# Optimization experiments

Measured on AMD Instinct MI355X. Metric: run time of the kernel, lower is better.

Reference implementation:

```python
import jax, jax.numpy as jnp
import numpy as np

SOS = 0
EOS = 1
NEG = -10000.0
B, S, T = 128, 1024, 128


def setup_inputs() -> dict:
    key = jax.random.key(0)
    k1, k2, k3 = jax.random.split(key, 3)
    emissions = jax.random.normal(k1, (B, S, T), dtype=jnp.float32)
    tags = jax.random.randint(k2, (B, S), 0, T)
    mask = jnp.ones((B, S), dtype=jnp.float32)
    transition = jax.random.uniform(k3, (T, T), minval=-0.1, maxval=0.1, dtype=jnp.float32)
    transition = transition.at[:, SOS].set(NEG).at[EOS, :].set(NEG)
    return {"emissions": emissions, "transition": transition, "mask": mask, "tags": tags}


def _crf_nll(emissions, transition, mask, tags):
    b, s, t = emissions.shape
    barange = jnp.arange(b)

    # ---- gold-path score (vectorized over time) ----
    first_tags = tags[:, 0]
    last_valid_idx = mask.astype(jnp.int32).sum(1) - 1
    last_tags = jnp.take_along_axis(tags, last_valid_idx[:, None], axis=1)[:, 0]

    score = transition[SOS, first_tags] + emissions[:, 0][barange, first_tags]
    e_scores = jnp.take_along_axis(emissions, tags[:, :, None], axis=2)[:, :, 0]  # (B,S)
    t_scores = transition[tags[:, :-1], tags[:, 1:]]                              # (B,S-1)
    score = score + ((e_scores[:, 1:] + t_scores) * mask[:, 1:]).sum(axis=1)
    score = score + transition[last_tags, EOS]

    # ---- log partition via forward algorithm (lax.scan over time) ----
    alphas0 = transition[SOS][None, :] + emissions[:, 0]  # (B,T)

    def step(alphas, inp):
        e_i, m_i = inp  # (B,T), (B,)
        # scores[b, prev, cur] = alphas[b, prev] + transition[prev, cur] + e_i[b, cur]
        scores = alphas[:, :, None] + transition[None, :, :] + e_i[:, None, :]
        new_alphas = jax.scipy.special.logsumexp(scores, axis=1)  # (B,T)
        m = m_i[:, None]
        return m * new_alphas + (1.0 - m) * alphas, None

    em_t = jnp.swapaxes(emissions, 0, 1)[1:]  # (S-1, B, T)
    mk_t = mask.T[1:]                         # (S-1, B)
    alphas, _ = jax.lax.scan(step, alphas0, (em_t, mk_t))

    partition = jax.scipy.special.logsumexp(alphas + transition[:, EOS][None, :], axis=1)  # (B,)
    return -jnp.sum(score - partition)


def reference(emissions, transition, mask, tags):
    return _crf_nll(emissions, transition, mask, tags)
```

## Files before the change

### kernel.cpp

```cpp
#include <hip/hip_runtime.h>
#include <cmath>

#define SOS 0
#define EOS 1
#define Bb 128
#define Ss 1024
#define Tt 128
#define LOG2E 1.4426950408889634f
#define LN2f  0.6931471805599453f

__global__ __launch_bounds__(256) void crf_forward(
    const float* __restrict__ em, const float* __restrict__ trans,
    const float* __restrict__ mask, float* __restrict__ part_out)
{
  __shared__ __align__(16) float s_trans[Tt * Tt];
  __shared__ __align__(16) float s_f[2][Tt];
  __shared__ __align__(16) float s_red[4];
  __shared__ __align__(16) float s_mask[Ss];

  const int tid = threadIdx.x;
  const int w   = tid >> 6;
  const int l   = tid & 63;
  const int jl  = l & 31;
  const int j   = w * 32 + jl;
  const int kh  = l >> 5;
  const int kbase = kh * 64;
  const int b   = blockIdx.x;
  const size_t base = (size_t)b * Ss * Tt;

  for (int i = tid; i < Ss; i += 256) s_mask[i] = mask[b * Ss + i];
  #pragma unroll
  for (int it = 0; it < 16; ++it) {
    int idx = (it * 256 + tid) * 4;
    *(float4*)&s_trans[idx] = *(const float4*)&trans[idx];
  }
  if (tid < 4) s_red[tid] = 0.5f;
  __syncthreads();

  float Mreg[64];
  #pragma unroll
  for (int kk = 0; kk < 64; ++kk)
    Mreg[kk] = exp2f(s_trans[(kbase + kk) * Tt + j] * LOG2E);
  const float tSOS  = s_trans[SOS * Tt + j];
  const float tEOS2 = s_trans[j * Tt + EOS] * LOG2E;

  float fn = exp2f((tSOS + em[base + j]) * LOG2E);
  if (l < 32) s_f[0][j] = fn;
  float c_scale = 0.f;
  float em0 = em[base + (size_t)1 * Tt + j];
  float em1 = em[base + (size_t)2 * Tt + j];
  __syncthreads();

  for (int i = 1; i < Ss; ++i) {
    const int p = i & 1;
    int ip = (i + 2 < Ss) ? (i + 2) : (Ss - 1);
    float em2 = em[base + (size_t)ip * Tt + j];
    float mi = s_mask[i];
    float fold = s_f[p ^ 1][j];

    float scl = 1.0f;
    if ((i & 3) == 1) {
      float4 r4 = *(float4*)&s_red[0];
      float M = fmaxf(fmaxf(r4.x, r4.y), fmaxf(r4.z, r4.w));
      int e; (void)frexpf(M, &e);
      scl = __int_as_float((127 - e) << 23);
      c_scale += (float)e;
    }
    float w_ = exp2f(em0 * LOG2E) * scl;

    float acc0 = 0.f, acc1 = 0.f, acc2 = 0.f, acc3 = 0.f;
    const float4* fsrc = (const float4*)&s_f[p ^ 1][kbase];
    #pragma unroll
    for (int q = 0; q < 16; ++q) {
      float4 fv = fsrc[q];
      acc0 = fmaf(fv.x, Mreg[4 * q + 0], acc0);
      acc1 = fmaf(fv.y, Mreg[4 * q + 1], acc1);
      acc2 = fmaf(fv.z, Mreg[4 * q + 2], acc2);
      acc3 = fmaf(fv.w, Mreg[4 * q + 3], acc3);
    }
    float g = (acc0 + acc1) + (acc2 + acc3);
    g += __shfl_xor(g, 32);

    float fnew = g * w_;
    fold *= scl;
    fn = (mi == 0.f) ? fold : fnew;
    if (l < 32) s_f[p][j] = fn;

    if ((i & 3) == 0) {
      float v = fn;
      #pragma unroll
      for (int o = 16; o > 0; o >>= 1) v = fmaxf(v, __shfl_xor(v, o));
      if (l == 0) s_red[w] = v;
    }
    em0 = em1; em1 = em2;
    __syncthreads();
  }

  float v = (l < 32) ? fn * exp2f(tEOS2) : 0.f;
  #pragma unroll
  for (int o = 32; o > 0; o >>= 1) v += __shfl_xor(v, o);
  if (l == 0) s_red[w] = v;
  __syncthreads();
  if (tid == 0) {
    float s = (s_red[0] + s_red[1]) + (s_red[2] + s_red[3]);
    part_out[b] = (log2f(s) + c_scale) * LN2f;
  }
}

__global__ __launch_bounds__(256) void crf_score(
    const float* __restrict__ em, const float* __restrict__ trans,
    const float* __restrict__ mask, const int* __restrict__ tags,
    float* __restrict__ sc)
{
  __shared__ float s_red[4];
  __shared__ float s_red2[4];
  const int tid = threadIdx.x;
  const int b = blockIdx.x;
  const size_t em_base = (size_t)b * Ss * Tt;
  const int* tg = tags + b * Ss;
  const float* mk = mask + b * Ss;

  float part = 0.f, msum = 0.f;
  for (int i = tid; i < Ss; i += 256) {
    float m = mk[i];
    msum += m;
    if (i >= 1) {
      int tc = tg[i], tp = tg[i - 1];
      part += m * (em[em_base + (size_t)i * Tt + tc] + trans[tp * Tt + tc]);
    }
  }
  #pragma unroll
  for (int o = 32; o > 0; o >>= 1) {
    part += __shfl_xor(part, o);
    msum += __shfl_xor(msum, o);
  }
  if ((tid & 63) == 0) { s_red[tid >> 6] = part; s_red2[tid >> 6] = msum; }
  __syncthreads();
  if (tid == 0) {
    float p  = s_red[0] + s_red[1] + s_red[2] + s_red[3];
    float ms = s_red2[0] + s_red2[1] + s_red2[2] + s_red2[3];
    int last = (int)(ms + 0.5f) - 1;
    int t0 = tg[0];
    float s = trans[SOS * Tt + t0] + em[em_base + t0] + p
            + trans[tg[last] * Tt + EOS];
    sc[b] = s;
  }
}

__global__ __launch_bounds__(128) void crf_combine(
    const float* __restrict__ part, const float* __restrict__ sc,
    float* __restrict__ out)
{
  __shared__ float s_red[2];
  const int tid = threadIdx.x;
  float v = part[tid] - sc[tid];
  #pragma unroll
  for (int o = 32; o > 0; o >>= 1) v += __shfl_xor(v, o);
  if ((tid & 63) == 0) s_red[tid >> 6] = v;
  __syncthreads();
  if (tid == 0) out[0] = s_red[0] + s_red[1];
}

extern "C" void kernel_launch(void* const* d_in, const int* in_sizes, int n_in,
                              void* d_out, int out_size, void* d_ws, size_t ws_size,
                              hipStream_t stream)
{
  const float* em    = (const float*)d_in[0];
  const float* trans = (const float*)d_in[1];
  const float* mask  = (const float*)d_in[2];
  const int*   tags  = (const int*)d_in[3];
  float* out = (float*)d_out;
  float* wsf = (float*)d_ws;
  float* part = wsf;
  float* sc   = wsf + 128;

  hipLaunchKernelGGL(crf_score, dim3(Bb), dim3(256), 0, stream,
                     em, trans, mask, tags, sc);
  hipLaunchKernelGGL(crf_forward, dim3(Bb), dim3(256), 0, stream,
                     em, trans, mask, part);
  hipLaunchKernelGGL(crf_combine, dim3(1), dim3(128), 0, stream,
                     part, sc, out);
}
```

Baseline: 543.3 us.

## Run CRF forward recurrence on a single wavefront with packed FMAs

Shrinks the forward kernel from four wavefronts to one 64-lane wavefront per sequence. Each lane keeps two output columns of the exponentiated transition matrix in registers and computes them with v_pk_fma_f32. This removes the per-step __syncthreads, the cross-half shuffle and the shared-memory max reduction, and the rescale max now uses only intra-wave shuffles. In exchange each lane does four times the multiply-adds per step, holds about 256 VGPRs of matrix data, and relies on LDS ordering within one wave for correctness.

```diff
diff --git a/kernel.cpp b/kernel.cpp
--- a/kernel.cpp
+++ b/kernel.cpp
@@ -9,102 +9,116 @@
 #define LOG2E 1.4426950408889634f
 #define LN2f  0.6931471805599453f
 
-__global__ __launch_bounds__(256) void crf_forward(
+typedef float f32x2 __attribute__((ext_vector_type(2)));
+typedef float f32x4 __attribute__((ext_vector_type(4)));
+
+__device__ __forceinline__ void pkfma(f32x2& acc, f32x2 a, f32x2 b) {
+  asm("v_pk_fma_f32 %0, %1, %2, %0" : "+v"(acc) : "v"(a), "v"(b));
+}
+
+template<int PH>
+__device__ __forceinline__ void crf_step(
+    int i, const float* __restrict__ em, size_t base, int j0,
+    float* s_f, const float* s_mask,
+    const f32x2 (&MA)[64], const f32x2 (&MB)[64],
+    f32x2& fprev, f32x2& pf, float& c_scale, float& nxt_scl, float& nxt_e)
+{
+  *(f32x2*)&s_f[j0] = fprev;
+  float mi = s_mask[i];
+  f32x2 emv = pf;
+  int r = (i + 4 < Ss) ? (i + 4) : (Ss - 1);
+  pf = *(const f32x2*)&em[base + (size_t)r * Tt + j0];
+
+  float sclv = 1.0f;
+  if constexpr (PH == 0) { sclv = nxt_scl; c_scale += nxt_e; }
+
+  f32x2 aA0 = {0.f, 0.f}, aA1 = {0.f, 0.f};
+  f32x2 aB0 = {0.f, 0.f}, aB1 = {0.f, 0.f};
+  const f32x4* fq = (const f32x4*)s_f;
+  #pragma unroll
+  for (int q = 0; q < 32; ++q) {
+    f32x4 v = fq[q];
+    f32x2 lo = __builtin_shufflevector(v, v, 0, 1);
+    f32x2 hi = __builtin_shufflevector(v, v, 2, 3);
+    pkfma(aA0, lo, MA[2 * q]);
+    pkfma(aA1, hi, MA[2 * q + 1]);
+    pkfma(aB0, lo, MB[2 * q]);
+    pkfma(aB1, hi, MB[2 * q + 1]);
+  }
+  f32x2 g;
+  g.x = (aA0.x + aA0.y) + (aA1.x + aA1.y);
+  g.y = (aB0.x + aB0.y) + (aB1.x + aB1.y);
+
+  f32x2 fn;
+  fn.x = g.x * (exp2f(emv.x * LOG2E) * sclv);
+  fn.y = g.y * (exp2f(emv.y * LOG2E) * sclv);
+  if (mi == 0.f) { fn.x = fprev.x * sclv; fn.y = fprev.y * sclv; }
+  fprev = fn;
+
+  if constexpr (PH == 3) {
+    float v = fmaxf(fn.x, fn.y);
+    #pragma unroll
+    for (int o = 32; o > 0; o >>= 1) v = fmaxf(v, __shfl_xor(v, o));
+    int e2; (void)frexpf(v, &e2);
+    nxt_scl = __int_as_float((127 - e2) << 23);
+    nxt_e = (float)e2;
+  }
+}
+
+__global__ __launch_bounds__(64, 1) void crf_forward(
     const float* __restrict__ em, const float* __restrict__ trans,
     const float* __restrict__ mask, float* __restrict__ part_out)
 {
-  __shared__ __align__(16) float s_trans[Tt * Tt];
-  __shared__ __align__(16) float s_f[2][Tt];
-  __shared__ __align__(16) float s_red[4];
+  __shared__ __align__(16) float s_f[Tt];
   __shared__ __align__(16) float s_mask[Ss];
 
-  const int tid = threadIdx.x;
-  const int w   = tid >> 6;
-  const int l   = tid & 63;
-  const int jl  = l & 31;
-  const int j   = w * 32 + jl;
-  const int kh  = l >> 5;
-  const int kbase = kh * 64;
-  const int b   = blockIdx.x;
+  const int l = threadIdx.x;
+  const int j0 = 2 * l;
+  const int b = blockIdx.x;
   const size_t base = (size_t)b * Ss * Tt;
 
-  for (int i = tid; i < Ss; i += 256) s_mask[i] = mask[b * Ss + i];
+  for (int i = l; i < Ss; i += 64) s_mask[i] = mask[b * Ss + i];
+
+  f32x2 MA[64], MB[64];
   #pragma unroll
-  for (int it = 0; it < 16; ++it) {
-    int idx = (it * 256 + tid) * 4;
-    *(float4*)&s_trans[idx] = *(const float4*)&trans[idx];
+  for (int k2 = 0; k2 < 64; ++k2) {
+    f32x2 r0 = *(const f32x2*)&trans[(2 * k2 + 0) * Tt + j0];
+    f32x2 r1 = *(const f32x2*)&trans[(2 * k2 + 1) * Tt + j0];
+    MA[k2] = f32x2{ exp2f(r0.x * LOG2E), exp2f(r1.x * LOG2E) };
+    MB[k2] = f32x2{ exp2f(r0.y * LOG2E), exp2f(r1.y * LOG2E) };
   }
-  if (tid < 4) s_red[tid] = 0.5f;
+  const f32x2 tS = *(const f32x2*)&trans[SOS * Tt + j0];
+  const float eA = exp2f(trans[(j0 + 0) * Tt + EOS] * LOG2E);
+  const float eB = exp2f(trans[(j0 + 1) * Tt + EOS] * LOG2E);
+
+  f32x2 e0 = *(const f32x2*)&em[base + j0];
+  f32x2 fprev;
+  fprev.x = exp2f((tS.x + e0.x) * LOG2E);
+  fprev.y = exp2f((tS.y + e0.y) * LOG2E);
+
+  f32x2 pf1 = *(const f32x2*)&em[base + (size_t)1 * Tt + j0];
+  f32x2 pf2 = *(const f32x2*)&em[base + (size_t)2 * Tt + j0];
+  f32x2 pf3 = *(const f32x2*)&em[base + (size_t)3 * Tt + j0];
+  f32x2 pf0 = *(const f32x2*)&em[base + (size_t)4 * Tt + j0];
+
+  float c_scale = 0.f, nxt_scl = 1.f, nxt_e = 0.f;
   __syncthreads();
 
-  float Mreg[64];
-  #pragma unroll
-  for (int kk = 0; kk < 64; ++kk)
-    Mreg[kk] = exp2f(s_trans[(kbase + kk) * Tt + j] * LOG2E);
-  const float tSOS  = s_trans[SOS * Tt + j];
-  const float tEOS2 = s_trans[j * Tt + EOS] * LOG2E;
+  int i = 1;
+  for (; i + 3 < Ss; i += 4) {
+    crf_step<1>(i + 0, em, base, j0, s_f, s_mask, MA, MB, fprev, pf1, c_scale, nxt_scl, nxt_e);
+    crf_step<2>(i + 1, em, base, j0, s_f, s_mask, MA, MB, fprev, pf2, c_scale, nxt_scl, nxt_e);
+    crf_step<3>(i + 2, em, base, j0, s_f, s_mask, MA, MB, fprev, pf3, c_scale, nxt_scl, nxt_e);
+    crf_step<0>(i + 3, em, base, j0, s_f, s_mask, MA, MB, fprev, pf0, c_scale, nxt_scl, nxt_e);
+  }
+  crf_step<1>(i + 0, em, base, j0, s_f, s_mask, MA, MB, fprev, pf1, c_scale, nxt_scl, nxt_e);
+  crf_step<2>(i + 1, em, base, j0, s_f, s_mask, MA, MB, fprev, pf2, c_scale, nxt_scl, nxt_e);
+  crf_step<3>(i + 2, em, base, j0, s_f, s_mask, MA, MB, fprev, pf3, c_scale, nxt_scl, nxt_e);
 
-  float fn = exp2f((tSOS + em[base + j]) * LOG2E);
-  if (l < 32) s_f[0][j] = fn;
-  float c_scale = 0.f;
-  float em0 = em[base + (size_t)1 * Tt + j];
-  float em1 = em[base + (size_t)2 * Tt + j];
-  __syncthreads();
-
-  for (int i = 1; i < Ss; ++i) {
-    const int p = i & 1;
-    int ip = (i + 2 < Ss) ? (i + 2) : (Ss - 1);
-    float em2 = em[base + (size_t)ip * Tt + j];
-    float mi = s_mask[i];
-    float fold = s_f[p ^ 1][j];
-
-    float scl = 1.0f;
-    if ((i & 3) == 1) {
-      float4 r4 = *(float4*)&s_red[0];
-      float M = fmaxf(fmaxf(r4.x, r4.y), fmaxf(r4.z, r4.w));
-      int e; (void)frexpf(M, &e);
-      scl = __int_as_float((127 - e) << 23);
-      c_scale += (float)e;
-    }
-    float w_ = exp2f(em0 * LOG2E) * scl;
-
-    float acc0 = 0.f, acc1 = 0.f, acc2 = 0.f, acc3 = 0.f;
-    const float4* fsrc = (const float4*)&s_f[p ^ 1][kbase];
-    #pragma unroll
-    for (int q = 0; q < 16; ++q) {
-      float4 fv = fsrc[q];
-      acc0 = fmaf(fv.x, Mreg[4 * q + 0], acc0);
-      acc1 = fmaf(fv.y, Mreg[4 * q + 1], acc1);
-      acc2 = fmaf(fv.z, Mreg[4 * q + 2], acc2);
-      acc3 = fmaf(fv.w, Mreg[4 * q + 3], acc3);
-    }
-    float g = (acc0 + acc1) + (acc2 + acc3);
-    g += __shfl_xor(g, 32);
-
-    float fnew = g * w_;
-    fold *= scl;
-    fn = (mi == 0.f) ? fold : fnew;
-    if (l < 32) s_f[p][j] = fn;
-
-    if ((i & 3) == 0) {
-      float v = fn;
-      #pragma unroll
-      for (int o = 16; o > 0; o >>= 1) v = fmaxf(v, __shfl_xor(v, o));
-      if (l == 0) s_red[w] = v;
-    }
-    em0 = em1; em1 = em2;
-    __syncthreads();
-  }
-
-  float v = (l < 32) ? fn * exp2f(tEOS2) : 0.f;
+  float v = fprev.x * eA + fprev.y * eB;
   #pragma unroll
   for (int o = 32; o > 0; o >>= 1) v += __shfl_xor(v, o);
-  if (l == 0) s_red[w] = v;
-  __syncthreads();
-  if (tid == 0) {
-    float s = (s_red[0] + s_red[1]) + (s_red[2] + s_red[3]);
-    part_out[b] = (log2f(s) + c_scale) * LN2f;
-  }
+  if (l == 0) part_out[b] = (log2f(v) + c_scale) * LN2f;
 }
 
 __global__ __launch_bounds__(256) void crf_score(
@@ -176,7 +190,7 @@
 
   hipLaunchKernelGGL(crf_score, dim3(Bb), dim3(256), 0, stream,
                      em, trans, mask, tags, sc);
-  hipLaunchKernelGGL(crf_forward, dim3(Bb), dim3(256), 0, stream,
+  hipLaunchKernelGGL(crf_forward, dim3(Bb), dim3(64), 0, stream,
                      em, trans, mask, part);
   hipLaunchKernelGGL(crf_combine, dim3(1), dim3(128), 0, stream,
                      part, sc, out);
```

Result: slower. 1.622 ms (+198.6%).

## Split CRF recursion into forward/backward halves using bf16 MFMA batched over sequences

Applied to the files above, without the earlier changes.

Replaces the per-sequence 256-thread FMA forward recursion with a forward-backward split: 32 blocks run the forward recursion over the first half of the sequence and 32 blocks run the backward recursion over the second half. Each block handles 4 sequences at once with the exp-transition matrix held in registers as bf16 MFMA fragments. A new combine kernel dots the alpha and beta vectors. This halves the serial chain length and turns the matvec into matrix-matrix MFMA work. In exchange it uses bf16 precision for the state and transition, runs only 64 single-wave blocks (low occupancy), and adds a kernel launch.

```diff
diff --git a/kernel.cpp b/kernel.cpp
--- a/kernel.cpp
+++ b/kernel.cpp
@@ -1,5 +1,6 @@
 #include <hip/hip_runtime.h>
 #include <cmath>
+#include <stdint.h>
 
 #define SOS 0
 #define EOS 1
@@ -9,102 +10,317 @@
 #define LOG2E 1.4426950408889634f
 #define LN2f  0.6931471805599453f
 
-__global__ __launch_bounds__(256) void crf_forward(
+typedef float  f32x2  __attribute__((ext_vector_type(2)));
+typedef float  f32x4  __attribute__((ext_vector_type(4)));
+typedef short  short4v __attribute__((ext_vector_type(4)));
+typedef short  short8v __attribute__((ext_vector_type(8)));
+
+#define WS_F    0
+#define WS_U    16384
+#define WS_CF   32768
+#define WS_CB   32896
+#define WS_PART 33024
+#define WS_SC   33152
+
+__device__ __forceinline__ unsigned short f2bf(float f) {
+  unsigned u = __float_as_uint(f);
+  return (unsigned short)((u + 0x7FFFu + ((u >> 16) & 1u)) >> 16);
+}
+__device__ __forceinline__ float bf2f(unsigned short h) {
+  return __uint_as_float(((unsigned)h) << 16);
+}
+__device__ __forceinline__ int sigma(int p) {
+  int t = p >> 4, cc = p & 15;
+  return 32 * (t & 3) + 2 * cc + (t >> 2);
+}
+
+template<int PH>
+__device__ __forceinline__ void crf_iter(
+    int it, bool fwd, int b0, int c, int g, bool allones,
+    const float* __restrict__ em, const float* __restrict__ mask,
+    unsigned short* y_s, float (&w_lds)[4][4][136],
+    const short8v (&Bf)[32],
+    f32x4& emE0, f32x4& emE1, f32x4& emO0, f32x4& emO1,
+    float& e_pend, f32x4& c4)
+{
+  constexpr int slot  = PH;
+  constexpr int slot2 = (PH + 2) & 3;
+  const unsigned ybase = (unsigned)(uintptr_t)y_s;
+
+  f32x2 wr[4][4];
+#pragma unroll
+  for (int m = 0; m < 4; ++m)
+#pragma unroll
+    for (int T = 0; T < 4; ++T)
+      wr[m][T] = *(const f32x2*)&w_lds[slot][m][32 * T + 2 * c];
+
+  asm volatile("s_waitcnt lgkmcnt(0)" ::: "memory");
+  short4v t0[4], t1[4];
+#pragma unroll
+  for (int kt = 0; kt < 4; ++kt) {
+    unsigned a1 = ybase + (unsigned)((32 * kt + 4 * g) * 32 + 2 * c);
+    asm volatile("ds_read_b64_tr_b16 %0, %1" : "=v"(t0[kt]) : "v"(a1));
+    asm volatile("ds_read_b64_tr_b16 %0, %1 offset:512" : "=v"(t1[kt]) : "v"(a1));
+  }
+  asm volatile("s_waitcnt lgkmcnt(0)" ::: "memory");
+  __builtin_amdgcn_sched_barrier(0);
+
+  short8v a8[4];
+#pragma unroll
+  for (int kt = 0; kt < 4; ++kt) {
+    short8v v;
+    v[0] = t0[kt][0]; v[1] = t0[kt][1]; v[2] = t0[kt][2]; v[3] = t0[kt][3];
+    v[4] = t1[kt][0]; v[5] = t1[kt][1]; v[6] = t1[kt][2]; v[7] = t1[kt][3];
+    a8[kt] = v;
+  }
+
+  f32x4 acc[8];
+#pragma unroll
+  for (int jt = 0; jt < 8; ++jt) acc[jt] = (f32x4){0.f, 0.f, 0.f, 0.f};
+#pragma unroll
+  for (int kt = 0; kt < 4; ++kt)
+#pragma unroll
+    for (int jt = 0; jt < 8; ++jt)
+      acc[jt] = __builtin_amdgcn_mfma_f32_16x16x32_bf16(a8[kt], Bf[kt * 8 + jt], acc[jt], 0, 0, 0);
+
+  {
+    f32x4 ea, eb2;
+    if constexpr (PH & 1) { ea = emO0; eb2 = emO1; } else { ea = emE0; eb2 = emE1; }
+    const float fold = (PH == 1) ? e_pend : 0.0f;
+    f32x4 wa, wb;
+#pragma unroll
+    for (int q = 0; q < 4; ++q) {
+      wa[q] = __builtin_amdgcn_exp2f(fmaf(ea[q],  LOG2E, -fold));
+      wb[q] = __builtin_amdgcn_exp2f(fmaf(eb2[q], LOG2E, -fold));
+    }
+    float* wp = &w_lds[slot2][g][8 * c];
+    *(f32x4*)wp = wa;
+    *(f32x4*)(wp + 4) = wb;
+    const int lr = fwd ? it + 4 : 1023 - it - 4;
+    const float* p = em + ((size_t)(b0 + g) * Ss + lr) * Tt + 8 * c;
+    f32x4 n0 = *(const f32x4*)p;
+    f32x4 n1 = *(const f32x4*)(p + 4);
+    if constexpr (PH & 1) { emO0 = n0; emO1 = n1; } else { emE0 = n0; emE1 = n1; }
+  }
+
+  float mloc = 0.0f;
+  f32x4 m4 = (f32x4){1.f, 1.f, 1.f, 1.f};
+  if (!allones) {
+    const int wrow = fwd ? it : 1023 - it;
+    m4[0] = mask[(size_t)(b0 + 0) * Ss + wrow];
+    m4[1] = mask[(size_t)(b0 + 1) * Ss + wrow];
+    m4[2] = mask[(size_t)(b0 + 2) * Ss + wrow];
+    m4[3] = mask[(size_t)(b0 + 3) * Ss + wrow];
+  }
+#pragma unroll
+  for (int jt = 0; jt < 8; ++jt) {
+    const int T = jt & 3, hi = jt >> 2;
+    float y0 = acc[jt][0] * wr[0][T][hi];
+    float y1 = acc[jt][1] * wr[1][T][hi];
+    float y2 = acc[jt][2] * wr[2][T][hi];
+    float y3 = acc[jt][3] * wr[3][T][hi];
+    if (!allones) {
+      short4v ov = *(short4v*)&y_s[(16 * jt + c) * 16];
+      if (m4[0] == 0.f) y0 = bf2f((unsigned short)ov[0]);
+      if (m4[1] == 0.f) y1 = bf2f((unsigned short)ov[1]);
+      if (m4[2] == 0.f) y2 = bf2f((unsigned short)ov[2]);
+      if (m4[3] == 0.f) y3 = bf2f((unsigned short)ov[3]);
+    }
+    if constexpr (PH == 0)
+      mloc = fmaxf(fmaxf(fmaxf(mloc, y0), fmaxf(y1, y2)), y3);
+    if (g == 0) {
+      short4v pk;
+      pk[0] = (short)f2bf(y0); pk[1] = (short)f2bf(y1);
+      pk[2] = (short)f2bf(y2); pk[3] = (short)f2bf(y3);
+      *(short4v*)&y_s[(16 * jt + c) * 16] = pk;
+    }
+  }
+  if constexpr (PH == 0) {
+#pragma unroll
+    for (int o = 1; o < 16; o <<= 1) mloc = fmaxf(mloc, __shfl_xor(mloc, o));
+    float g0 = __shfl(mloc, c);
+    int ei = (int)((__float_as_uint(g0) >> 23) & 255u) - 127;
+    e_pend = (float)ei;
+  }
+  if constexpr (PH == 3) {
+    if (allones) {
+      c4[0] += e_pend; c4[1] += e_pend; c4[2] += e_pend; c4[3] += e_pend;
+    } else {
+      c4[0] += (m4[0] != 0.f) ? e_pend : 0.f;
+      c4[1] += (m4[1] != 0.f) ? e_pend : 0.f;
+      c4[2] += (m4[2] != 0.f) ? e_pend : 0.f;
+      c4[3] += (m4[3] != 0.f) ? e_pend : 0.f;
+    }
+  }
+}
+
+__global__ __launch_bounds__(64) void crf_fb(
     const float* __restrict__ em, const float* __restrict__ trans,
-    const float* __restrict__ mask, float* __restrict__ part_out)
+    const float* __restrict__ mask, float* __restrict__ wsf)
 {
   __shared__ __align__(16) float s_trans[Tt * Tt];
-  __shared__ __align__(16) float s_f[2][Tt];
-  __shared__ __align__(16) float s_red[4];
-  __shared__ __align__(16) float s_mask[Ss];
-
-  const int tid = threadIdx.x;
-  const int w   = tid >> 6;
-  const int l   = tid & 63;
-  const int jl  = l & 31;
-  const int j   = w * 32 + jl;
-  const int kh  = l >> 5;
-  const int kbase = kh * 64;
-  const int b   = blockIdx.x;
-  const size_t base = (size_t)b * Ss * Tt;
-
-  for (int i = tid; i < Ss; i += 256) s_mask[i] = mask[b * Ss + i];
-  #pragma unroll
-  for (int it = 0; it < 16; ++it) {
-    int idx = (it * 256 + tid) * 4;
-    *(float4*)&s_trans[idx] = *(const float4*)&trans[idx];
-  }
-  if (tid < 4) s_red[tid] = 0.5f;
-  __syncthreads();
-
-  float Mreg[64];
-  #pragma unroll
-  for (int kk = 0; kk < 64; ++kk)
-    Mreg[kk] = exp2f(s_trans[(kbase + kk) * Tt + j] * LOG2E);
-  const float tSOS  = s_trans[SOS * Tt + j];
-  const float tEOS2 = s_trans[j * Tt + EOS] * LOG2E;
-
-  float fn = exp2f((tSOS + em[base + j]) * LOG2E);
-  if (l < 32) s_f[0][j] = fn;
-  float c_scale = 0.f;
-  float em0 = em[base + (size_t)1 * Tt + j];
-  float em1 = em[base + (size_t)2 * Tt + j];
-  __syncthreads();
-
-  for (int i = 1; i < Ss; ++i) {
-    const int p = i & 1;
-    int ip = (i + 2 < Ss) ? (i + 2) : (Ss - 1);
-    float em2 = em[base + (size_t)ip * Tt + j];
-    float mi = s_mask[i];
-    float fold = s_f[p ^ 1][j];
-
-    float scl = 1.0f;
-    if ((i & 3) == 1) {
-      float4 r4 = *(float4*)&s_red[0];
-      float M = fmaxf(fmaxf(r4.x, r4.y), fmaxf(r4.z, r4.w));
-      int e; (void)frexpf(M, &e);
-      scl = __int_as_float((127 - e) << 23);
-      c_scale += (float)e;
-    }
-    float w_ = exp2f(em0 * LOG2E) * scl;
-
-    float acc0 = 0.f, acc1 = 0.f, acc2 = 0.f, acc3 = 0.f;
-    const float4* fsrc = (const float4*)&s_f[p ^ 1][kbase];
-    #pragma unroll
-    for (int q = 0; q < 16; ++q) {
-      float4 fv = fsrc[q];
-      acc0 = fmaf(fv.x, Mreg[4 * q + 0], acc0);
-      acc1 = fmaf(fv.y, Mreg[4 * q + 1], acc1);
-      acc2 = fmaf(fv.z, Mreg[4 * q + 2], acc2);
-      acc3 = fmaf(fv.w, Mreg[4 * q + 3], acc3);
-    }
-    float g = (acc0 + acc1) + (acc2 + acc3);
-    g += __shfl_xor(g, 32);
-
-    float fnew = g * w_;
-    fold *= scl;
-    fn = (mi == 0.f) ? fold : fnew;
-    if (l < 32) s_f[p][j] = fn;
-
-    if ((i & 3) == 0) {
-      float v = fn;
-      #pragma unroll
-      for (int o = 16; o > 0; o >>= 1) v = fmaxf(v, __shfl_xor(v, o));
-      if (l == 0) s_red[w] = v;
-    }
-    em0 = em1; em1 = em2;
-    __syncthreads();
-  }
-
-  float v = (l < 32) ? fn * exp2f(tEOS2) : 0.f;
-  #pragma unroll
-  for (int o = 32; o > 0; o >>= 1) v += __shfl_xor(v, o);
-  if (l == 0) s_red[w] = v;
-  __syncthreads();
-  if (tid == 0) {
-    float s = (s_red[0] + s_red[1]) + (s_red[2] + s_red[3]);
-    part_out[b] = (log2f(s) + c_scale) * LN2f;
-  }
+  __shared__ __align__(16) unsigned short y_s[128 * 16];
+  __shared__ __align__(16) float w_lds[4][4][136];
+
+  const int l = threadIdx.x, c = l & 15, g = l >> 4;
+  const int bk = blockIdx.x;
+  const bool fwd = bk < 32;
+  const int b0 = (fwd ? bk : bk - 32) * 4;
+  const unsigned ybase = (unsigned)(uintptr_t)y_s;
+
+  for (int itr = 0; itr < 64; ++itr)
+    ((f32x4*)s_trans)[itr * 64 + l] = ((const f32x4*)trans)[itr * 64 + l];
+
+  short8v Bf[32];
+#pragma unroll
+  for (int jt = 0; jt < 8; ++jt) {
+    asm volatile("s_waitcnt lgkmcnt(0)" ::: "memory");
+#pragma unroll
+    for (int rr = 0; rr < 2; ++rr) {
+      const int k = l + rr * 64;
+#pragma unroll
+      for (int nn4 = 0; nn4 < 4; ++nn4) {
+        short4v pk;
+#pragma unroll
+        for (int q = 0; q < 4; ++q) {
+          const int nn = nn4 * 4 + q, n = 16 * jt + nn;
+          const int ia = fwd ? sigma(k) : sigma(n);
+          const int ib = fwd ? sigma(n) : sigma(k);
+          pk[q] = (short)f2bf(__builtin_amdgcn_exp2f(s_trans[ia * Tt + ib] * LOG2E));
+        }
+        *(short4v*)&y_s[k * 16 + nn4 * 4] = pk;
+      }
+    }
+    asm volatile("s_waitcnt lgkmcnt(0)" ::: "memory");
+#pragma unroll
+    for (int kt = 0; kt < 4; ++kt) {
+      unsigned a1 = ybase + (unsigned)((32 * kt + 4 * g) * 32 + 2 * c);
+      short4v u0, u1;
+      asm volatile("ds_read_b64_tr_b16 %0, %1" : "=v"(u0) : "v"(a1));
+      asm volatile("ds_read_b64_tr_b16 %0, %1 offset:512" : "=v"(u1) : "v"(a1));
+      asm volatile("s_waitcnt lgkmcnt(0)" ::: "memory");
+      short8v v;
+      v[0] = u0[0]; v[1] = u0[1]; v[2] = u0[2]; v[3] = u0[3];
+      v[4] = u1[0]; v[5] = u1[1]; v[6] = u1[2]; v[7] = u1[3];
+      Bf[kt * 8 + jt] = v;
+    }
+  }
+
+  {
+    short4v z = (short4v){0, 0, 0, 0};
+#pragma unroll
+    for (int rr = 0; rr < 2; ++rr) {
+      const int k = l + rr * 64;
+#pragma unroll
+      for (int nn4 = 0; nn4 < 4; ++nn4) *(short4v*)&y_s[k * 16 + nn4 * 4] = z;
+    }
+  }
+
+  if (g == 0) {
+#pragma unroll
+    for (int t = 0; t < 8; ++t) {
+      const int p = 16 * t + c, j = sigma(p);
+      short4v pk;
+#pragma unroll
+      for (int m = 0; m < 4; ++m) {
+        float x;
+        if (fwd) x = (s_trans[SOS * Tt + j] + em[((size_t)(b0 + m) * Ss) * Tt + j]) * LOG2E;
+        else     x = s_trans[j * Tt + EOS] * LOG2E;
+        pk[m] = (short)f2bf(__builtin_amdgcn_exp2f(x));
+      }
+      *(short4v*)&y_s[p * 16] = pk;
+    }
+  }
+
+  float mn = 1.0f;
+  for (int r = 0; r < 4; ++r)
+    for (int idx = l; idx < Ss; idx += 64)
+      mn = fminf(mn, mask[(size_t)(b0 + r) * Ss + idx]);
+#pragma unroll
+  for (int o = 1; o < 64; o <<= 1) mn = fminf(mn, __shfl_xor(mn, o));
+  const bool allones = (mn == 1.0f);
+
+  const int i0 = fwd ? 1 : 0;
+#pragma unroll
+  for (int s = 0; s < 2; ++s) {
+    const int itw = i0 + s;
+    const int row = fwd ? itw : 1023 - itw;
+    const int sl = itw & 3;
+    const float* p = em + ((size_t)(b0 + g) * Ss + row) * Tt + 8 * c;
+    f32x4 a = *(const f32x4*)p, b = *(const f32x4*)(p + 4);
+    f32x4 wa, wb;
+#pragma unroll
+    for (int q = 0; q < 4; ++q) {
+      wa[q] = __builtin_amdgcn_exp2f(a[q] * LOG2E);
+      wb[q] = __builtin_amdgcn_exp2f(b[q] * LOG2E);
+    }
+    float* wp = &w_lds[sl][g][8 * c];
+    *(f32x4*)wp = wa; *(f32x4*)(wp + 4) = wb;
+  }
+  f32x4 emE0, emE1, emO0, emO1;
+  {
+    const int itA = i0 + 2, itB = i0 + 3;
+    const int rowA = fwd ? itA : 1023 - itA;
+    const int rowB = fwd ? itB : 1023 - itB;
+    const float* pA = em + ((size_t)(b0 + g) * Ss + rowA) * Tt + 8 * c;
+    const float* pB = em + ((size_t)(b0 + g) * Ss + rowB) * Tt + 8 * c;
+    if ((itA & 1) == 0) {
+      emE0 = *(const f32x4*)pA; emE1 = *(const f32x4*)(pA + 4);
+      emO0 = *(const f32x4*)pB; emO1 = *(const f32x4*)(pB + 4);
+    } else {
+      emO0 = *(const f32x4*)pA; emO1 = *(const f32x4*)(pA + 4);
+      emE0 = *(const f32x4*)pB; emE1 = *(const f32x4*)(pB + 4);
+    }
+  }
+
+  float e_pend = 0.f;
+  f32x4 c4 = (f32x4){0.f, 0.f, 0.f, 0.f};
+
+#define ARGS fwd, b0, c, g, allones, em, mask, y_s, w_lds, Bf, emE0, emE1, emO0, emO1, e_pend, c4
+  if (fwd) {
+    int i = 1;
+    for (int blk = 0; blk < 127; ++blk) {
+      crf_iter<1>(i, ARGS); crf_iter<2>(i + 1, ARGS);
+      crf_iter<3>(i + 2, ARGS); crf_iter<0>(i + 3, ARGS);
+      i += 4;
+    }
+    crf_iter<1>(509, ARGS); crf_iter<2>(510, ARGS); crf_iter<3>(511, ARGS);
+  } else {
+    int n = 0;
+    for (int blk = 0; blk < 128; ++blk) {
+      crf_iter<0>(n, ARGS); crf_iter<1>(n + 1, ARGS);
+      crf_iter<2>(n + 2, ARGS); crf_iter<3>(n + 3, ARGS);
+      n += 4;
+    }
+  }
+#undef ARGS
+
+  asm volatile("s_waitcnt lgkmcnt(0)" ::: "memory");
+  const int so = fwd ? WS_F : WS_U;
+#pragma unroll
+  for (int rr = 0; rr < 2; ++rr) {
+    const int p = l + rr * 64;
+    short4v v = *(short4v*)&y_s[p * 16];
+#pragma unroll
+    for (int m = 0; m < 4; ++m)
+      wsf[so + (b0 + m) * 128 + p] = bf2f((unsigned short)v[m]);
+  }
+  if (l == 0) {
+    float* cp = wsf + (fwd ? WS_CF : WS_CB);
+    cp[b0 + 0] = c4[0]; cp[b0 + 1] = c4[1];
+    cp[b0 + 2] = c4[2]; cp[b0 + 3] = c4[3];
+  }
+}
+
+__global__ __launch_bounds__(64) void crf_combine1(float* __restrict__ wsf)
+{
+  const int b = blockIdx.x, l = threadIdx.x;
+  float a = wsf[WS_F + b * 128 + l]      * wsf[WS_U + b * 128 + l]
+          + wsf[WS_F + b * 128 + 64 + l] * wsf[WS_U + b * 128 + 64 + l];
+#pragma unroll
+  for (int o = 32; o > 0; o >>= 1) a += __shfl_xor(a, o);
+  if (l == 0)
+    wsf[WS_PART + b] = (log2f(a) + wsf[WS_CF + b] + wsf[WS_CB + b]) * LN2f;
 }
 
 __global__ __launch_bounds__(256) void crf_score(
@@ -129,7 +345,7 @@
       part += m * (em[em_base + (size_t)i * Tt + tc] + trans[tp * Tt + tc]);
     }
   }
-  #pragma unroll
+#pragma unroll
   for (int o = 32; o > 0; o >>= 1) {
     part += __shfl_xor(part, o);
     msum += __shfl_xor(msum, o);
@@ -147,14 +363,13 @@
   }
 }
 
-__global__ __launch_bounds__(128) void crf_combine(
-    const float* __restrict__ part, const float* __restrict__ sc,
-    float* __restrict__ out)
+__global__ __launch_bounds__(128) void crf_final(
+    const float* __restrict__ wsf, float* __restrict__ out)
 {
   __shared__ float s_red[2];
   const int tid = threadIdx.x;
-  float v = part[tid] - sc[tid];
-  #pragma unroll
+  float v = wsf[WS_PART + tid] - wsf[WS_SC + tid];
+#pragma unroll
   for (int o = 32; o > 0; o >>= 1) v += __shfl_xor(v, o);
   if ((tid & 63) == 0) s_red[tid >> 6] = v;
   __syncthreads();
@@ -171,13 +386,11 @@
   const int*   tags  = (const int*)d_in[3];
   float* out = (float*)d_out;
   float* wsf = (float*)d_ws;
-  float* part = wsf;
-  float* sc   = wsf + 128;
 
   hipLaunchKernelGGL(crf_score, dim3(Bb), dim3(256), 0, stream,
-                     em, trans, mask, tags, sc);
-  hipLaunchKernelGGL(crf_forward, dim3(Bb), dim3(256), 0, stream,
-                     em, trans, mask, part);
-  hipLaunchKernelGGL(crf_combine, dim3(1), dim3(128), 0, stream,
-                     part, sc, out);
-}
+                     em, trans, mask, tags, wsf + WS_SC);
+  hipLaunchKernelGGL(crf_fb, dim3(64), dim3(64), 0, stream,
+                     em, trans, mask, wsf);
+  hipLaunchKernelGGL(crf_combine1, dim3(Bb), dim3(64), 0, stream, wsf);
+  hipLaunchKernelGGL(crf_final, dim3(1), dim3(128), 0, stream, wsf, out);
+}
```

Result: slower. 556.7 us (+2.5%).
